# Kernel tuning notes

Hardware: AMD Instinct MI355X
Metric: run time of the kernel (lower is better)

Reference implementation:

```python
import jax, jax.numpy as jnp
import numpy as np

WS = 11          # window_size
SIGMA = 1.5
PAD = (WS - 1) // 2
C1 = (0.01 * 1.0) ** 2
C2 = (0.03 * 1.0) ** 2


def _gaussian_kernel2d():
    # kornia-style: 1D gaussian over window, normalized, outer product
    x = jnp.arange(WS, dtype=jnp.float32) - WS // 2
    g = jnp.exp(-(x ** 2) / (2.0 * SIGMA ** 2))
    g = g / jnp.sum(g)
    return jnp.outer(g, g)  # [WS, WS]


def _filter2d(x, k2d):
    # depthwise 2D filter with reflect ('same') padding, as kornia.filter2D
    b, c, h, w = x.shape
    xp = jnp.pad(x, ((0, 0), (0, 0), (PAD, PAD), (PAD, PAD)), mode='reflect')
    kern = jnp.broadcast_to(k2d.astype(x.dtype), (c, 1, WS, WS))
    return jax.lax.conv_general_dilated(
        xp, kern, window_strides=(1, 1), padding='VALID',
        feature_group_count=c,
        dimension_numbers=('NCHW', 'OIHW', 'NCHW'))


def setup_inputs() -> dict:
    key = jax.random.key(0)
    k1, k2 = jax.random.split(key)
    inp = jax.random.normal(k1, (16, 1, 1024, 1024), dtype=jnp.float32)
    tgt = jax.random.uniform(k2, (16, 1, 1024, 1024), dtype=jnp.float32)
    return {"input": inp, "target": tgt}


def reference(input, target):
    k2d = _gaussian_kernel2d()
    img1 = jax.nn.sigmoid(input)  # logsigmoid(x).exp() == sigmoid(x)
    img2 = target

    mu1 = _filter2d(img1, k2d)
    mu2 = _filter2d(img2, k2d)
    mu1_sq = mu1 * mu1
    mu2_sq = mu2 * mu2
    mu1_mu2 = mu1 * mu2

    sigma1_sq = _filter2d(img1 * img1, k2d) - mu1_sq
    sigma2_sq = _filter2d(img2 * img2, k2d) - mu2_sq
    sigma12 = _filter2d(img1 * img2, k2d) - mu1_mu2

    ssim_map = ((2.0 * mu1_mu2 + C1) * (2.0 * sigma12 + C2)) / (
        (mu1_sq + mu2_sq + C1) * (sigma1_sq + sigma2_sq + C2))
    loss = jnp.clip(1.0 - ssim_map, 0.0, 1.0) / 2.0
    return jnp.mean(loss)  # reduction='mean'
```

## Files before the change

### kernel.cpp

```cpp
#include <hip/hip_runtime.h>
#include <math.h>


typedef __attribute__((ext_vector_type(2))) float f2;

#define H_IMG 1024
#define W_IMG 1024
#define N_IMG 16
#define WAVE_W 64
#define TILE_H 128
#define PADR 5
#define LDS_S2 76

constexpr float GW[11] = {
    0.00102838f, 0.00759877f, 0.03600077f, 0.10936069f, 0.21300553f,
    0.26601172f,
    0.21300553f, 0.10936069f, 0.03600077f, 0.00759877f, 0.00102838f};

__device__ __forceinline__ int reflect_i(int i, int n) {
    i = (i < 0) ? -i : i;
    i = (i >= n) ? (2 * n - 2 - i) : i;
    return i;
}

__device__ __forceinline__ float fast_sigmoid(float x) {
    return __builtin_amdgcn_rcpf(1.0f + __expf(-x));
}

__device__ __forceinline__ void ssim_emit(
    f2 mu, f2 sx, float& loss_sum)
{
    const float mu1 = mu.x, mu2 = mu.y;
    const float mu1s = mu1 * mu1;
    const float mu2s = mu2 * mu2;
    const float mu12 = mu1 * mu2;
    const float ssum = sx.x - mu1s - mu2s;
    const float s12  = sx.y - mu12;
    const float C1 = 1e-4f, C2 = 9e-4f;
    const float num = (2.0f * mu12 + C1) * (2.0f * s12 + C2);
    const float den = (mu1s + mu2s + C1) * (ssum + C2);
    float l = 1.0f - num * __builtin_amdgcn_rcpf(den);
    l = fminf(fmaxf(l, 0.0f), 1.0f) * 0.5f;
    loss_sum += l;
}

template<int NR>
__device__ __forceinline__ void load_group(
    const float* __restrict__ A, const float* __restrict__ B,
    int y_start, int gb, int c0, int c1, int lane,
    float (&pa)[11], float (&pb)[11], float (&pa2)[11], float (&pb2)[11])
{
#pragma unroll
    for (int r = 0; r < NR; ++r) {
        const int yy = reflect_i(y_start + gb + r, H_IMG);
        const size_t ro = (size_t)yy << 10;
        pa[r] = A[ro + c0];
        pb[r] = B[ro + c0];
        if (lane < 2 * PADR) {
            pa2[r] = A[ro + c1];
            pb2[r] = B[ro + c1];
        }
    }
}

template<int NR>
__device__ __forceinline__ void write_group(
    f2 (*__restrict__ buf)[LDS_S2], int lane,
    const float (&pa)[11], const float (&pb)[11],
    const float (&pa2)[11], const float (&pb2)[11])
{
#pragma unroll
    for (int r = 0; r < NR; ++r) {
        buf[r][lane] = (f2){fast_sigmoid(pa[r]), pb[r]};
        if (lane < 2 * PADR)
            buf[r][WAVE_W + lane] = (f2){fast_sigmoid(pa2[r]), pb2[r]};
    }
}

template<int NR, bool GUARD>
__device__ __forceinline__ void process_group(
    const f2 (*__restrict__ buf)[LDS_S2], int lane,
    f2 (&vAB)[11], f2 (&vSX)[11], float& loss_sum)
{
#pragma unroll
    for (int r = 0; r < NR; ++r) {
        f2 hAB = (f2)(0.0f), hSQ = (f2)(0.0f);
        float hab = 0.0f;
#pragma unroll
        for (int k = 0; k < 11; ++k) {
            const f2 v   = buf[r][lane + k];
            const f2 wa2 = ((f2)(GW[k])) * v;
            hAB += wa2;
            hSQ  = __builtin_elementwise_fma(wa2, v, hSQ);
            hab  = fmaf(wa2.x, v.y, hab);
        }
        const f2 hSX = (f2){hSQ.x + hSQ.y, hab};
#pragma unroll
        for (int j = 0; j < 11; ++j) {
            if (!(GUARD && j > r)) {
                const int s = (r - j + 22) % 11;
                const f2 w2 = (f2)(GW[j]);
                vAB[s] = __builtin_elementwise_fma(w2, hAB, vAB[s]);
                vSX[s] = __builtin_elementwise_fma(w2, hSX, vSX[s]);
            }
        }
        if (!GUARD || r == 10) {
            const int s = (r + 1) % 11;
            ssim_emit(vAB[s], vSX[s], loss_sum);
            vAB[s] = (f2)(0.0f); vSX[s] = (f2)(0.0f);
        }
    }
}

__global__ __launch_bounds__(256, 2) void ssim_main(
    const float* __restrict__ inp, const float* __restrict__ tgt,
    float* __restrict__ out)
{
    __shared__ f2 lds[4][2][11][LDS_S2];
    __shared__ float red[4];

    const int tid  = threadIdx.x;
    const int lane = tid & 63;
    const int w    = tid >> 6;
    const int blk  = blockIdx.x;
    const int b    = blk >> 5;
    const int rem  = blk & 31;
    const int ry   = rem >> 2;
    const int cs   = (rem & 3) * 4 + w;
    const int x0   = cs * WAVE_W;
    const int y0   = ry * TILE_H;

    const float* __restrict__ A = inp + (size_t)b * (H_IMG * (size_t)W_IMG);
    const float* __restrict__ B = tgt + (size_t)b * (H_IMG * (size_t)W_IMG);

    const int c0 = reflect_i(x0 - PADR + lane, W_IMG);
    const int c1 = (lane < 2 * PADR)
                       ? reflect_i(x0 + WAVE_W - PADR + lane, W_IMG) : 0;

    f2 vAB[11], vSX[11];
#pragma unroll
    for (int j = 0; j < 11; ++j) {
        vAB[j] = (f2)(0.0f); vSX[j] = (f2)(0.0f);
    }
    float pa[11], pb[11], pa2[11], pb2[11];
    float loss_sum = 0.0f;

    const int y_start = y0 - PADR;

    load_group<11>(A, B, y_start, 0, c0, c1, lane, pa, pb, pa2, pb2);
    write_group<11>(lds[w][0], lane, pa, pb, pa2, pb2);
    load_group<11>(A, B, y_start, 11, c0, c1, lane, pa, pb, pa2, pb2);
    process_group<11, true>(lds[w][0], lane, vAB, vSX, loss_sum);

#pragma unroll 1
    for (int g = 1; g <= 11; ++g) {
        f2 (*cur)[LDS_S2] = lds[w][g & 1];
        write_group<11>(cur, lane, pa, pb, pa2, pb2);
        if (g <= 10)
            load_group<11>(A, B, y_start, (g + 1) * 11, c0, c1, lane,
                           pa, pb, pa2, pb2);
        else
            load_group<6>(A, B, y_start, 132, c0, c1, lane,
                          pa, pb, pa2, pb2);
        process_group<11, false>(cur, lane, vAB, vSX, loss_sum);
    }

    write_group<6>(lds[w][0], lane, pa, pb, pa2, pb2);
    process_group<6, false>(lds[w][0], lane, vAB, vSX, loss_sum);

#pragma unroll
    for (int off = 32; off > 0; off >>= 1)
        loss_sum += __shfl_down(loss_sum, off, 64);
    if (lane == 0) red[w] = loss_sum;
    __syncthreads();
    if (tid == 0) {
        const float s = red[0] + red[1] + red[2] + red[3];
        atomicAdd(out, s * (1.0f / ((float)N_IMG * H_IMG * W_IMG)));
    }
}

extern "C" void kernel_launch(void* const* d_in, const int* in_sizes, int n_in,
                              void* d_out, int out_size, void* d_ws, size_t ws_size,
                              hipStream_t stream) {
    const float* inp = (const float*)d_in[0];
    const float* tgt = (const float*)d_in[1];
    float* out = (float*)d_out;

    hipMemsetAsync(out, 0, sizeof(float), stream);

    const int grid = N_IMG * 4 * (H_IMG / TILE_H);
    ssim_main<<<grid, 256, 0, stream>>>(inp, tgt, out);
}
```

Measured before the change: 183.2 us.

## Precompute squared and cross products into LDS and specialize interior tiles

```diff
diff --git a/kernel.cpp b/kernel.cpp
--- a/kernel.cpp
+++ b/kernel.cpp
@@ -2,7 +2,7 @@
 #include <math.h>
 
 
-typedef __attribute__((ext_vector_type(2))) float f2;
+typedef __attribute__((ext_vector_type(4))) float f4;
 
 #define H_IMG 1024
 #define W_IMG 1024
@@ -10,7 +10,7 @@
 #define WAVE_W 64
 #define TILE_H 128
 #define PADR 5
-#define LDS_S2 76
+#define LDS_S4 76
 
 constexpr float GW[11] = {
     0.00102838f, 0.00759877f, 0.03600077f, 0.10936069f, 0.21300553f,
@@ -28,14 +28,13 @@
 }
 
 __device__ __forceinline__ void ssim_emit(
-    f2 mu, f2 sx, float& loss_sum)
-{
-    const float mu1 = mu.x, mu2 = mu.y;
+    float mu1, float mu2, float ss, float pp, float& loss_sum)
+{
     const float mu1s = mu1 * mu1;
     const float mu2s = mu2 * mu2;
     const float mu12 = mu1 * mu2;
-    const float ssum = sx.x - mu1s - mu2s;
-    const float s12  = sx.y - mu12;
+    const float ssum = ss - mu1s - mu2s;
+    const float s12  = pp - mu12;
     const float C1 = 1e-4f, C2 = 9e-4f;
     const float num = (2.0f * mu12 + C1) * (2.0f * s12 + C2);
     const float den = (mu1s + mu2s + C1) * (ssum + C2);
@@ -44,7 +43,7 @@
     loss_sum += l;
 }
 
-template<int NR>
+template<int NR, bool EDGE>
 __device__ __forceinline__ void load_group(
     const float* __restrict__ A, const float* __restrict__ B,
     int y_start, int gb, int c0, int c1, int lane,
@@ -52,7 +51,8 @@
 {
 #pragma unroll
     for (int r = 0; r < NR; ++r) {
-        const int yy = reflect_i(y_start + gb + r, H_IMG);
+        const int yr = y_start + gb + r;
+        const int yy = EDGE ? reflect_i(yr, H_IMG) : yr;
         const size_t ro = (size_t)yy << 10;
         pa[r] = A[ro + c0];
         pb[r] = B[ro + c0];
@@ -65,58 +65,99 @@
 
 template<int NR>
 __device__ __forceinline__ void write_group(
-    f2 (*__restrict__ buf)[LDS_S2], int lane,
+    f4 (*__restrict__ buf)[LDS_S4], int lane,
     const float (&pa)[11], const float (&pb)[11],
     const float (&pa2)[11], const float (&pb2)[11])
 {
 #pragma unroll
     for (int r = 0; r < NR; ++r) {
-        buf[r][lane] = (f2){fast_sigmoid(pa[r]), pb[r]};
-        if (lane < 2 * PADR)
-            buf[r][WAVE_W + lane] = (f2){fast_sigmoid(pa2[r]), pb2[r]};
+        {
+            const float a = fast_sigmoid(pa[r]);
+            const float b = pb[r];
+            buf[r][lane] = (f4){a, b, fmaf(a, a, b * b), a * b};
+        }
+        if (lane < 2 * PADR) {
+            const float a = fast_sigmoid(pa2[r]);
+            const float b = pb2[r];
+            buf[r][WAVE_W + lane] = (f4){a, b, fmaf(a, a, b * b), a * b};
+        }
     }
 }
 
 template<int NR, bool GUARD>
 __device__ __forceinline__ void process_group(
-    const f2 (*__restrict__ buf)[LDS_S2], int lane,
-    f2 (&vAB)[11], f2 (&vSX)[11], float& loss_sum)
+    const f4 (*__restrict__ buf)[LDS_S4], int lane,
+    float (&va)[11], float (&vb)[11], float (&vs_)[11], float (&vp)[11],
+    float& loss_sum)
 {
 #pragma unroll
     for (int r = 0; r < NR; ++r) {
-        f2 hAB = (f2)(0.0f), hSQ = (f2)(0.0f);
-        float hab = 0.0f;
+        float hA = 0.0f, hB = 0.0f, hS = 0.0f, hP = 0.0f;
 #pragma unroll
         for (int k = 0; k < 11; ++k) {
-            const f2 v   = buf[r][lane + k];
-            const f2 wa2 = ((f2)(GW[k])) * v;
-            hAB += wa2;
-            hSQ  = __builtin_elementwise_fma(wa2, v, hSQ);
-            hab  = fmaf(wa2.x, v.y, hab);
-        }
-        const f2 hSX = (f2){hSQ.x + hSQ.y, hab};
+            const f4 v = buf[r][lane + k];
+            hA = fmaf(GW[k], v.x, hA);
+            hB = fmaf(GW[k], v.y, hB);
+            hS = fmaf(GW[k], v.z, hS);
+            hP = fmaf(GW[k], v.w, hP);
+        }
 #pragma unroll
         for (int j = 0; j < 11; ++j) {
             if (!(GUARD && j > r)) {
                 const int s = (r - j + 22) % 11;
-                const f2 w2 = (f2)(GW[j]);
-                vAB[s] = __builtin_elementwise_fma(w2, hAB, vAB[s]);
-                vSX[s] = __builtin_elementwise_fma(w2, hSX, vSX[s]);
+                va[s]  = fmaf(GW[j], hA, va[s]);
+                vb[s]  = fmaf(GW[j], hB, vb[s]);
+                vs_[s] = fmaf(GW[j], hS, vs_[s]);
+                vp[s]  = fmaf(GW[j], hP, vp[s]);
             }
         }
         if (!GUARD || r == 10) {
             const int s = (r + 1) % 11;
-            ssim_emit(vAB[s], vSX[s], loss_sum);
-            vAB[s] = (f2)(0.0f); vSX[s] = (f2)(0.0f);
-        }
-    }
+            ssim_emit(va[s], vb[s], vs_[s], vp[s], loss_sum);
+            va[s] = 0.0f; vb[s] = 0.0f; vs_[s] = 0.0f; vp[s] = 0.0f;
+        }
+    }
+}
+
+template<bool EDGE>
+__device__ __forceinline__ void run_tile(
+    const float* __restrict__ A, const float* __restrict__ B,
+    int y_start, int c0, int c1, int lane,
+    f4 (*__restrict__ buf)[LDS_S4], float& loss_sum)
+{
+    float va[11], vb[11], vs_[11], vp[11];
+#pragma unroll
+    for (int j = 0; j < 11; ++j) {
+        va[j] = 0.0f; vb[j] = 0.0f; vs_[j] = 0.0f; vp[j] = 0.0f;
+    }
+    float pa[11], pb[11], pa2[11], pb2[11];
+
+    load_group<11, EDGE>(A, B, y_start, 0, c0, c1, lane, pa, pb, pa2, pb2);
+    write_group<11>(buf, lane, pa, pb, pa2, pb2);
+    load_group<11, EDGE>(A, B, y_start, 11, c0, c1, lane, pa, pb, pa2, pb2);
+    process_group<11, true>(buf, lane, va, vb, vs_, vp, loss_sum);
+
+#pragma unroll 1
+    for (int g = 1; g <= 11; ++g) {
+        write_group<11>(buf, lane, pa, pb, pa2, pb2);
+        if (g <= 10)
+            load_group<11, EDGE>(A, B, y_start, (g + 1) * 11, c0, c1, lane,
+                                 pa, pb, pa2, pb2);
+        else
+            load_group<6, EDGE>(A, B, y_start, 132, c0, c1, lane,
+                                pa, pb, pa2, pb2);
+        process_group<11, false>(buf, lane, va, vb, vs_, vp, loss_sum);
+    }
+
+    write_group<6>(buf, lane, pa, pb, pa2, pb2);
+    process_group<6, false>(buf, lane, va, vb, vs_, vp, loss_sum);
 }
 
 __global__ __launch_bounds__(256, 2) void ssim_main(
     const float* __restrict__ inp, const float* __restrict__ tgt,
     float* __restrict__ out)
 {
-    __shared__ f2 lds[4][2][11][LDS_S2];
+    __shared__ f4 lds[4][11][LDS_S4];
     __shared__ float red[4];
 
     const int tid  = threadIdx.x;
@@ -137,36 +178,13 @@
     const int c1 = (lane < 2 * PADR)
                        ? reflect_i(x0 + WAVE_W - PADR + lane, W_IMG) : 0;
 
-    f2 vAB[11], vSX[11];
-#pragma unroll
-    for (int j = 0; j < 11; ++j) {
-        vAB[j] = (f2)(0.0f); vSX[j] = (f2)(0.0f);
-    }
-    float pa[11], pb[11], pa2[11], pb2[11];
     float loss_sum = 0.0f;
-
     const int y_start = y0 - PADR;
 
-    load_group<11>(A, B, y_start, 0, c0, c1, lane, pa, pb, pa2, pb2);
-    write_group<11>(lds[w][0], lane, pa, pb, pa2, pb2);
-    load_group<11>(A, B, y_start, 11, c0, c1, lane, pa, pb, pa2, pb2);
-    process_group<11, true>(lds[w][0], lane, vAB, vSX, loss_sum);
-
-#pragma unroll 1
-    for (int g = 1; g <= 11; ++g) {
-        f2 (*cur)[LDS_S2] = lds[w][g & 1];
-        write_group<11>(cur, lane, pa, pb, pa2, pb2);
-        if (g <= 10)
-            load_group<11>(A, B, y_start, (g + 1) * 11, c0, c1, lane,
-                           pa, pb, pa2, pb2);
-        else
-            load_group<6>(A, B, y_start, 132, c0, c1, lane,
-                          pa, pb, pa2, pb2);
-        process_group<11, false>(cur, lane, vAB, vSX, loss_sum);
-    }
-
-    write_group<6>(lds[w][0], lane, pa, pb, pa2, pb2);
-    process_group<6, false>(lds[w][0], lane, vAB, vSX, loss_sum);
+    if (ry == 0 || ry == 7)
+        run_tile<true>(A, B, y_start, c0, c1, lane, lds[w], loss_sum);
+    else
+        run_tile<false>(A, B, y_start, c0, c1, lane, lds[w], loss_sum);
 
 #pragma unroll
     for (int off = 32; off > 0; off >>= 1)
```

Result: slower. 259.8 us (+41.9%).

## Halve tile height, single-buffer LDS, and specialize interior tiles without reflect

Applied to the files above, without the earlier changes.

```diff
diff --git a/kernel.cpp b/kernel.cpp
--- a/kernel.cpp
+++ b/kernel.cpp
@@ -8,7 +8,7 @@
 #define W_IMG 1024
 #define N_IMG 16
 #define WAVE_W 64
-#define TILE_H 128
+#define TILE_H 64
 #define PADR 5
 #define LDS_S2 76
 
@@ -44,7 +44,7 @@
     loss_sum += l;
 }
 
-template<int NR>
+template<int NR, bool EDGE>
 __device__ __forceinline__ void load_group(
     const float* __restrict__ A, const float* __restrict__ B,
     int y_start, int gb, int c0, int c1, int lane,
@@ -52,7 +52,8 @@
 {
 #pragma unroll
     for (int r = 0; r < NR; ++r) {
-        const int yy = reflect_i(y_start + gb + r, H_IMG);
+        const int yr = y_start + gb + r;
+        const int yy = EDGE ? reflect_i(yr, H_IMG) : yr;
         const size_t ro = (size_t)yy << 10;
         pa[r] = A[ro + c0];
         pb[r] = B[ro + c0];
@@ -112,19 +113,53 @@
     }
 }
 
+template<bool EDGE>
+__device__ __forceinline__ void run_tile(
+    const float* __restrict__ A, const float* __restrict__ B,
+    int y_start, int c0, int c1, int lane,
+    f2 (*__restrict__ buf)[LDS_S2], float& loss_sum)
+{
+    f2 vAB[11], vSX[11];
+#pragma unroll
+    for (int j = 0; j < 11; ++j) {
+        vAB[j] = (f2)(0.0f); vSX[j] = (f2)(0.0f);
+    }
+    float pa[11], pb[11], pa2[11], pb2[11];
+
+    load_group<11, EDGE>(A, B, y_start, 0, c0, c1, lane, pa, pb, pa2, pb2);
+    write_group<11>(buf, lane, pa, pb, pa2, pb2);
+    load_group<11, EDGE>(A, B, y_start, 11, c0, c1, lane, pa, pb, pa2, pb2);
+    process_group<11, true>(buf, lane, vAB, vSX, loss_sum);
+
+#pragma unroll 1
+    for (int g = 1; g <= 5; ++g) {
+        write_group<11>(buf, lane, pa, pb, pa2, pb2);
+        if (g <= 4)
+            load_group<11, EDGE>(A, B, y_start, (g + 1) * 11, c0, c1, lane,
+                                 pa, pb, pa2, pb2);
+        else
+            load_group<8, EDGE>(A, B, y_start, 66, c0, c1, lane,
+                                pa, pb, pa2, pb2);
+        process_group<11, false>(buf, lane, vAB, vSX, loss_sum);
+    }
+
+    write_group<8>(buf, lane, pa, pb, pa2, pb2);
+    process_group<8, false>(buf, lane, vAB, vSX, loss_sum);
+}
+
 __global__ __launch_bounds__(256, 2) void ssim_main(
     const float* __restrict__ inp, const float* __restrict__ tgt,
     float* __restrict__ out)
 {
-    __shared__ f2 lds[4][2][11][LDS_S2];
+    __shared__ f2 lds[4][11][LDS_S2];
     __shared__ float red[4];
 
     const int tid  = threadIdx.x;
     const int lane = tid & 63;
     const int w    = tid >> 6;
     const int blk  = blockIdx.x;
-    const int b    = blk >> 5;
-    const int rem  = blk & 31;
+    const int b    = blk >> 6;
+    const int rem  = blk & 63;
     const int ry   = rem >> 2;
     const int cs   = (rem & 3) * 4 + w;
     const int x0   = cs * WAVE_W;
@@ -137,36 +172,13 @@
     const int c1 = (lane < 2 * PADR)
                        ? reflect_i(x0 + WAVE_W - PADR + lane, W_IMG) : 0;
 
-    f2 vAB[11], vSX[11];
-#pragma unroll
-    for (int j = 0; j < 11; ++j) {
-        vAB[j] = (f2)(0.0f); vSX[j] = (f2)(0.0f);
-    }
-    float pa[11], pb[11], pa2[11], pb2[11];
     float loss_sum = 0.0f;
-
     const int y_start = y0 - PADR;
 
-    load_group<11>(A, B, y_start, 0, c0, c1, lane, pa, pb, pa2, pb2);
-    write_group<11>(lds[w][0], lane, pa, pb, pa2, pb2);
-    load_group<11>(A, B, y_start, 11, c0, c1, lane, pa, pb, pa2, pb2);
-    process_group<11, true>(lds[w][0], lane, vAB, vSX, loss_sum);
-
-#pragma unroll 1
-    for (int g = 1; g <= 11; ++g) {
-        f2 (*cur)[LDS_S2] = lds[w][g & 1];
-        write_group<11>(cur, lane, pa, pb, pa2, pb2);
-        if (g <= 10)
-            load_group<11>(A, B, y_start, (g + 1) * 11, c0, c1, lane,
-                           pa, pb, pa2, pb2);
-        else
-            load_group<6>(A, B, y_start, 132, c0, c1, lane,
-                          pa, pb, pa2, pb2);
-        process_group<11, false>(cur, lane, vAB, vSX, loss_sum);
-    }
-
-    write_group<6>(lds[w][0], lane, pa, pb, pa2, pb2);
-    process_group<6, false>(lds[w][0], lane, vAB, vSX, loss_sum);
+    if (ry == 0 || ry == 15)
+        run_tile<true>(A, B, y_start, c0, c1, lane, lds[w], loss_sum);
+    else
+        run_tile<false>(A, B, y_start, c0, c1, lane, lds[w], loss_sum);
 
 #pragma unroll
     for (int off = 32; off > 0; off >>= 1)
```

Result: slower. 191.0 us (+4.3%).
